# Kernel tuning notes

Hardware: AMD Instinct MI355X
Metric: run time of the kernel (lower is better)

## Reference

```python
import jax, jax.numpy as jnp
import numpy as np

N_NODES = 10000
N_EDGES = 640000
D_FEAT = 128
N_CLASSES = 40


def setup_inputs() -> dict:
    key = jax.random.key(0)
    k1, k2, k3, k4 = jax.random.split(key, 4)
    x = jax.random.normal(k1, (N_NODES, D_FEAT), dtype=jnp.float32)
    edge_index = jax.random.randint(k2, (2, N_EDGES), 0, N_NODES, dtype=jnp.int64)
    # SAGEConv params: lin_l (neighbor path, with bias), lin_r (root path, no bias)
    W_l = jax.random.normal(k3, (D_FEAT, N_CLASSES), dtype=jnp.float32) / np.sqrt(D_FEAT)
    b_l = jnp.zeros((N_CLASSES,), dtype=jnp.float32)
    W_r = jax.random.normal(k4, (D_FEAT, N_CLASSES), dtype=jnp.float32) / np.sqrt(D_FEAT)
    return {"x": x, "edge_index": edge_index, "W_l": W_l, "b_l": b_l, "W_r": W_r}


def reference(x, edge_index, W_l, b_l, W_r):
    # SAGEConv(aggr='max'): gather source features, scatter-max into destinations
    src, dst = edge_index[0], edge_index[1]
    msgs = x[src]                                        # [E, F] gather
    agg = jax.ops.segment_max(msgs, dst, num_segments=x.shape[0])  # [N, F]
    # nodes with no incoming edges: PyG fills with 0
    agg = jnp.where(jnp.isneginf(agg), 0.0, agg)
    out = agg @ W_l + b_l + x @ W_r                      # [N, C]
    return jax.nn.log_softmax(out, axis=1)
```

## Files before the change

### kernel.cpp

```cpp
#include <hip/hip_runtime.h>
#include <hip/hip_bf16.h>
#include <math.h>

#define D_FEAT 128
#define N_CLASSES 40
#define CAP 128

#define CNT_PAD_INTS (10000 * 16)
#define XB_BYTES (10000 * D_FEAT * 2)
#define CNT_BYTES (CNT_PAD_INTS * 4)

typedef int v4i __attribute__((ext_vector_type(4)));


extern "C" __global__ void __launch_bounds__(256)
gnn_cvt(const float* __restrict__ x, __hip_bfloat16* __restrict__ xb,
        int* __restrict__ cnt, int n4)
{
    int t = blockIdx.x * 256 + threadIdx.x;
    if (t < CNT_PAD_INTS / 4) {
        reinterpret_cast<v4i*>(cnt)[t] = (v4i){0, 0, 0, 0};
    }
    if (t >= n4) return;
    float4 v = reinterpret_cast<const float4*>(x)[t];
    __hip_bfloat16 o[4];
    o[0] = __float2bfloat16(v.x);
    o[1] = __float2bfloat16(v.y);
    o[2] = __float2bfloat16(v.z);
    o[3] = __float2bfloat16(v.w);
    *reinterpret_cast<uint2*>(xb + (size_t)t * 4) = *reinterpret_cast<uint2*>(o);
}

extern "C" __global__ void __launch_bounds__(256)
gnn_bucketize(const int* __restrict__ src, const int* __restrict__ dst,
              int* __restrict__ cnt, unsigned short* __restrict__ bucket,
              int n_edges4)
{
    int t = blockIdx.x * 256 + threadIdx.x;
    if (t >= n_edges4) return;
    v4i s4 = __builtin_nontemporal_load(reinterpret_cast<const v4i*>(src) + t);
    v4i d4 = __builtin_nontemporal_load(reinterpret_cast<const v4i*>(dst) + t);
    int p0 = atomicAdd(&cnt[d4.x << 4], 1);
    int p1 = atomicAdd(&cnt[d4.y << 4], 1);
    int p2 = atomicAdd(&cnt[d4.z << 4], 1);
    int p3 = atomicAdd(&cnt[d4.w << 4], 1);
    if (p0 < CAP) bucket[(size_t)d4.x * CAP + p0] = (unsigned short)s4.x;
    if (p1 < CAP) bucket[(size_t)d4.y * CAP + p1] = (unsigned short)s4.y;
    if (p2 < CAP) bucket[(size_t)d4.z * CAP + p2] = (unsigned short)s4.z;
    if (p3 < CAP) bucket[(size_t)d4.w * CAP + p3] = (unsigned short)s4.w;
}

extern "C" __global__ void __launch_bounds__(256)
gnn_fused(const float* __restrict__ x, const __hip_bfloat16* __restrict__ xb,
          const int* __restrict__ cnt, const unsigned short* __restrict__ bucket,
          const float* __restrict__ W_l, const float* __restrict__ b_l,
          const float* __restrict__ W_r,
          float* __restrict__ out, int n_nodes)
{
    __shared__ float sa[4][D_FEAT];
    __shared__ float sx[4][D_FEAT];

    const int wave = threadIdx.x >> 6;
    const int lane = threadIdx.x & 63;
    const int node = blockIdx.x * 4 + wave;
    const bool valid = (node < n_nodes);

    const int sub = lane >> 4;
    const int q   = lane & 15;
    const int c8  = q * 8;

    int deg = 0;
    if (valid) deg = min(cnt[node << 4], CAP);

    float acc[8];
    #pragma unroll
    for (int i = 0; i < 8; ++i) acc[i] = -INFINITY;

    const unsigned short* brow = bucket + (size_t)node * CAP;

    for (int base = 0; base < deg; base += 64) {
        const int nb = min(64, deg - base);
        int myid = brow[base + min(lane, nb - 1)];

        if (nb == 64) {
            #pragma unroll
            for (int k = 0; k < 64; k += 16) {
                int ss[4];
                #pragma unroll
                for (int j = 0; j < 4; ++j) ss[j] = __shfl(myid, k + 4 * j + sub, 64);
                uint4 vv[4];
                #pragma unroll
                for (int j = 0; j < 4; ++j)
                    vv[j] = *reinterpret_cast<const uint4*>(xb + (size_t)ss[j] * D_FEAT + c8);
                #pragma unroll
                for (int j = 0; j < 4; ++j) {
                    const unsigned int* u = &vv[j].x;
                    #pragma unroll
                    for (int w = 0; w < 4; ++w) {
                        acc[2*w]   = fmaxf(acc[2*w],   __uint_as_float(u[w] << 16));
                        acc[2*w+1] = fmaxf(acc[2*w+1], __uint_as_float(u[w] & 0xffff0000u));
                    }
                }
            }
        } else {
            for (int k = 0; k < nb; k += 8) {
                int e0 = min(k + sub, nb - 1);
                int e1 = min(k + 4 + sub, nb - 1);
                int s0 = __shfl(myid, e0, 64);
                int s1 = __shfl(myid, e1, 64);
                uint4 v0 = *reinterpret_cast<const uint4*>(xb + (size_t)s0 * D_FEAT + c8);
                uint4 v1 = *reinterpret_cast<const uint4*>(xb + (size_t)s1 * D_FEAT + c8);
                const unsigned int* u0 = &v0.x;
                const unsigned int* u1 = &v1.x;
                #pragma unroll
                for (int w = 0; w < 4; ++w) {
                    acc[2*w]   = fmaxf(acc[2*w],   __uint_as_float(u0[w] << 16));
                    acc[2*w+1] = fmaxf(acc[2*w+1], __uint_as_float(u0[w] & 0xffff0000u));
                    acc[2*w]   = fmaxf(acc[2*w],   __uint_as_float(u1[w] << 16));
                    acc[2*w+1] = fmaxf(acc[2*w+1], __uint_as_float(u1[w] & 0xffff0000u));
                }
            }
        }
    }

    #pragma unroll
    for (int i = 0; i < 8; ++i) {
        acc[i] = fmaxf(acc[i], __shfl_xor(acc[i], 16, 64));
        acc[i] = fmaxf(acc[i], __shfl_xor(acc[i], 32, 64));
    }
    if (deg == 0) {
        #pragma unroll
        for (int i = 0; i < 8; ++i) acc[i] = 0.0f;
    }

    if (valid) {
        if (sub == 0) {
            #pragma unroll
            for (int i = 0; i < 8; ++i) sa[wave][c8 + i] = acc[i];
        }
        if (lane < 32) {
            *reinterpret_cast<float4*>(&sx[wave][lane * 4]) =
                *reinterpret_cast<const float4*>(x + (size_t)node * D_FEAT + lane * 4);
        }
    }

    float o = 0.0f;
    if (valid && lane < N_CLASSES) {
        o = b_l[lane];
        #pragma unroll 8
        for (int f = 0; f < D_FEAT; ++f) {
            o = fmaf(sa[wave][f], W_l[f * N_CLASSES + lane], o);
            o = fmaf(sx[wave][f], W_r[f * N_CLASSES + lane], o);
        }
    }

    float mm = (valid && lane < N_CLASSES) ? o : -INFINITY;
    #pragma unroll
    for (int off = 32; off > 0; off >>= 1) mm = fmaxf(mm, __shfl_xor(mm, off, 64));
    float ex = (valid && lane < N_CLASSES) ? expf(o - mm) : 0.0f;
    float ss = ex;
    #pragma unroll
    for (int off = 32; off > 0; off >>= 1) ss += __shfl_xor(ss, off, 64);

    if (valid && lane < N_CLASSES)
        out[(size_t)node * N_CLASSES + lane] = o - mm - logf(ss);
}

extern "C" void kernel_launch(void* const* d_in, const int* in_sizes, int n_in,
                              void* d_out, int out_size, void* d_ws, size_t ws_size,
                              hipStream_t stream) {
    const float* x   = (const float*)d_in[0];
    const int*   ei  = (const int*)d_in[1];
    const float* W_l = (const float*)d_in[2];
    const float* b_l = (const float*)d_in[3];
    const float* W_r = (const float*)d_in[4];
    float* out = (float*)d_out;

    const int n_nodes = in_sizes[0] / D_FEAT;
    const int n_edges = in_sizes[1] / 2;
    const int* src = ei;
    const int* dst = ei + n_edges;

    char* w = (char*)d_ws;
    __hip_bfloat16* xb = (__hip_bfloat16*)w;
    int* cnt = (int*)(w + XB_BYTES);
    unsigned short* bucket = (unsigned short*)(w + XB_BYTES + CNT_BYTES);

    {
        int n4 = n_nodes * D_FEAT / 4;
        int blocks = (n4 + 255) / 256;
        gnn_cvt<<<blocks, 256, 0, stream>>>(x, xb, cnt, n4);
    }
    {
        int n_edges4 = n_edges / 4;
        int blocks = (n_edges4 + 255) / 256;
        gnn_bucketize<<<blocks, 256, 0, stream>>>(src, dst, cnt, bucket, n_edges4);
    }
    {
        int blocks = (n_nodes + 3) / 4;
        gnn_fused<<<blocks, 256, 0, stream>>>(x, xb, cnt, bucket, W_l, b_l, W_r,
                                              out, n_nodes);
    }
}
```

Baseline: 70.07 us.

## Switch gathered features to fp16 with packed max and dot2 projection

```diff
diff --git a/kernel.cpp b/kernel.cpp
--- a/kernel.cpp
+++ b/kernel.cpp
@@ -1,5 +1,4 @@
 #include <hip/hip_runtime.h>
-#include <hip/hip_bf16.h>
 #include <math.h>
 
 #define D_FEAT 128
@@ -7,28 +6,50 @@
 #define CAP 128
 
 #define CNT_PAD_INTS (10000 * 16)
-#define XB_BYTES (10000 * D_FEAT * 2)
+#define XH_BYTES (10000 * D_FEAT * 2)
 #define CNT_BYTES (CNT_PAD_INTS * 4)
+#define WPK_U32 (64 * N_CLASSES)
 
 typedef int v4i __attribute__((ext_vector_type(4)));
+typedef _Float16 h2 __attribute__((ext_vector_type(2)));
+
+static __device__ __forceinline__ unsigned int pkmax(unsigned int a, unsigned int b) {
+    unsigned int d;
+    asm("v_pk_max_f16 %0, %1, %2" : "=v"(d) : "v"(a), "v"(b));
+    return d;
+}
+static __device__ __forceinline__ float fdot2(unsigned int a, unsigned int b, float c) {
+    return __builtin_amdgcn_fdot2(__builtin_bit_cast(h2, a),
+                                  __builtin_bit_cast(h2, b), c, false);
+}
+static __device__ __forceinline__ unsigned short f2h(float f) {
+    return __builtin_bit_cast(unsigned short, (_Float16)f);
+}
 
 
 extern "C" __global__ void __launch_bounds__(256)
-gnn_cvt(const float* __restrict__ x, __hip_bfloat16* __restrict__ xb,
-        int* __restrict__ cnt, int n4)
+gnn_cvt(const float* __restrict__ x, unsigned int* __restrict__ xh,
+        int* __restrict__ cnt,
+        const float* __restrict__ W_l, const float* __restrict__ W_r,
+        unsigned int* __restrict__ Wlpk, unsigned int* __restrict__ Wrpk, int n4)
 {
     int t = blockIdx.x * 256 + threadIdx.x;
     if (t < CNT_PAD_INTS / 4) {
         reinterpret_cast<v4i*>(cnt)[t] = (v4i){0, 0, 0, 0};
     }
+    if (t < WPK_U32) {
+        int f2 = t / N_CLASSES, c = t % N_CLASSES;
+        Wlpk[t] = (unsigned int)f2h(W_l[(2 * f2) * N_CLASSES + c])
+                | ((unsigned int)f2h(W_l[(2 * f2 + 1) * N_CLASSES + c]) << 16);
+        Wrpk[t] = (unsigned int)f2h(W_r[(2 * f2) * N_CLASSES + c])
+                | ((unsigned int)f2h(W_r[(2 * f2 + 1) * N_CLASSES + c]) << 16);
+    }
     if (t >= n4) return;
     float4 v = reinterpret_cast<const float4*>(x)[t];
-    __hip_bfloat16 o[4];
-    o[0] = __float2bfloat16(v.x);
-    o[1] = __float2bfloat16(v.y);
-    o[2] = __float2bfloat16(v.z);
-    o[3] = __float2bfloat16(v.w);
-    *reinterpret_cast<uint2*>(xb + (size_t)t * 4) = *reinterpret_cast<uint2*>(o);
+    uint2 o;
+    o.x = (unsigned int)f2h(v.x) | ((unsigned int)f2h(v.y) << 16);
+    o.y = (unsigned int)f2h(v.z) | ((unsigned int)f2h(v.w) << 16);
+    reinterpret_cast<uint2*>(xh)[t] = o;
 }
 
 extern "C" __global__ void __launch_bounds__(256)
@@ -51,14 +72,14 @@
 }
 
 extern "C" __global__ void __launch_bounds__(256)
-gnn_fused(const float* __restrict__ x, const __hip_bfloat16* __restrict__ xb,
+gnn_fused(const unsigned int* __restrict__ xh,
           const int* __restrict__ cnt, const unsigned short* __restrict__ bucket,
-          const float* __restrict__ W_l, const float* __restrict__ b_l,
-          const float* __restrict__ W_r,
+          const unsigned int* __restrict__ Wlpk, const unsigned int* __restrict__ Wrpk,
+          const float* __restrict__ b_l,
           float* __restrict__ out, int n_nodes)
 {
-    __shared__ float sa[4][D_FEAT];
-    __shared__ float sx[4][D_FEAT];
+    __shared__ unsigned int sa2[4][64];
+    __shared__ unsigned int sx2[4][64];
 
     const int wave = threadIdx.x >> 6;
     const int lane = threadIdx.x & 63;
@@ -67,16 +88,16 @@
 
     const int sub = lane >> 4;
     const int q   = lane & 15;
-    const int c8  = q * 8;
 
     int deg = 0;
     if (valid) deg = min(cnt[node << 4], CAP);
 
-    float acc[8];
-    #pragma unroll
-    for (int i = 0; i < 8; ++i) acc[i] = -INFINITY;
+    unsigned int acc2[4];
+    #pragma unroll
+    for (int i = 0; i < 4; ++i) acc2[i] = 0xFC00FC00u;
 
     const unsigned short* brow = bucket + (size_t)node * CAP;
+    const uint4* xh4 = reinterpret_cast<const uint4*>(xh);
 
     for (int base = 0; base < deg; base += 64) {
         const int nb = min(64, deg - base);
@@ -90,16 +111,12 @@
                 for (int j = 0; j < 4; ++j) ss[j] = __shfl(myid, k + 4 * j + sub, 64);
                 uint4 vv[4];
                 #pragma unroll
-                for (int j = 0; j < 4; ++j)
-                    vv[j] = *reinterpret_cast<const uint4*>(xb + (size_t)ss[j] * D_FEAT + c8);
+                for (int j = 0; j < 4; ++j) vv[j] = xh4[ss[j] * 16 + q];
                 #pragma unroll
                 for (int j = 0; j < 4; ++j) {
                     const unsigned int* u = &vv[j].x;
                     #pragma unroll
-                    for (int w = 0; w < 4; ++w) {
-                        acc[2*w]   = fmaxf(acc[2*w],   __uint_as_float(u[w] << 16));
-                        acc[2*w+1] = fmaxf(acc[2*w+1], __uint_as_float(u[w] & 0xffff0000u));
-                    }
+                    for (int w = 0; w < 4; ++w) acc2[w] = pkmax(acc2[w], u[w]);
                 }
             }
         } else {
@@ -108,49 +125,57 @@
                 int e1 = min(k + 4 + sub, nb - 1);
                 int s0 = __shfl(myid, e0, 64);
                 int s1 = __shfl(myid, e1, 64);
-                uint4 v0 = *reinterpret_cast<const uint4*>(xb + (size_t)s0 * D_FEAT + c8);
-                uint4 v1 = *reinterpret_cast<const uint4*>(xb + (size_t)s1 * D_FEAT + c8);
+                uint4 v0 = xh4[s0 * 16 + q];
+                uint4 v1 = xh4[s1 * 16 + q];
                 const unsigned int* u0 = &v0.x;
                 const unsigned int* u1 = &v1.x;
                 #pragma unroll
                 for (int w = 0; w < 4; ++w) {
-                    acc[2*w]   = fmaxf(acc[2*w],   __uint_as_float(u0[w] << 16));
-                    acc[2*w+1] = fmaxf(acc[2*w+1], __uint_as_float(u0[w] & 0xffff0000u));
-                    acc[2*w]   = fmaxf(acc[2*w],   __uint_as_float(u1[w] << 16));
-                    acc[2*w+1] = fmaxf(acc[2*w+1], __uint_as_float(u1[w] & 0xffff0000u));
+                    acc2[w] = pkmax(acc2[w], u0[w]);
+                    acc2[w] = pkmax(acc2[w], u1[w]);
                 }
             }
         }
     }
 
     #pragma unroll
-    for (int i = 0; i < 8; ++i) {
-        acc[i] = fmaxf(acc[i], __shfl_xor(acc[i], 16, 64));
-        acc[i] = fmaxf(acc[i], __shfl_xor(acc[i], 32, 64));
+    for (int i = 0; i < 4; ++i) {
+        acc2[i] = pkmax(acc2[i], (unsigned int)__shfl_xor((int)acc2[i], 16, 64));
+        acc2[i] = pkmax(acc2[i], (unsigned int)__shfl_xor((int)acc2[i], 32, 64));
     }
     if (deg == 0) {
         #pragma unroll
-        for (int i = 0; i < 8; ++i) acc[i] = 0.0f;
+        for (int i = 0; i < 4; ++i) acc2[i] = 0u;
     }
 
     if (valid) {
         if (sub == 0) {
-            #pragma unroll
-            for (int i = 0; i < 8; ++i) sa[wave][c8 + i] = acc[i];
-        }
-        if (lane < 32) {
-            *reinterpret_cast<float4*>(&sx[wave][lane * 4]) =
-                *reinterpret_cast<const float4*>(x + (size_t)node * D_FEAT + lane * 4);
+            uint4 w4;
+            w4.x = acc2[0]; w4.y = acc2[1]; w4.z = acc2[2]; w4.w = acc2[3];
+            *reinterpret_cast<uint4*>(&sa2[wave][q * 4]) = w4;
+        }
+        if (lane < 16) {
+            reinterpret_cast<uint4*>(sx2[wave])[lane] = xh4[node * 16 + lane];
         }
     }
 
     float o = 0.0f;
     if (valid && lane < N_CLASSES) {
         o = b_l[lane];
-        #pragma unroll 8
-        for (int f = 0; f < D_FEAT; ++f) {
-            o = fmaf(sa[wave][f], W_l[f * N_CLASSES + lane], o);
-            o = fmaf(sx[wave][f], W_r[f * N_CLASSES + lane], o);
+        const uint4* a4 = reinterpret_cast<const uint4*>(sa2[wave]);
+        const uint4* x4 = reinterpret_cast<const uint4*>(sx2[wave]);
+        #pragma unroll 4
+        for (int i = 0; i < 16; ++i) {
+            uint4 a  = a4[i];
+            uint4 xx = x4[i];
+            const unsigned int* ua = &a.x;
+            const unsigned int* ux = &xx.x;
+            #pragma unroll
+            for (int j = 0; j < 4; ++j) {
+                int f2 = i * 4 + j;
+                o = fdot2(ua[j], Wlpk[f2 * N_CLASSES + lane], o);
+                o = fdot2(ux[j], Wrpk[f2 * N_CLASSES + lane], o);
+            }
         }
     }
 
@@ -182,14 +207,17 @@
     const int* dst = ei + n_edges;
 
     char* w = (char*)d_ws;
-    __hip_bfloat16* xb = (__hip_bfloat16*)w;
-    int* cnt = (int*)(w + XB_BYTES);
-    unsigned short* bucket = (unsigned short*)(w + XB_BYTES + CNT_BYTES);
+    unsigned int* xh = (unsigned int*)w;
+    int* cnt = (int*)(w + XH_BYTES);
+    unsigned int* Wlpk = (unsigned int*)(w + XH_BYTES + CNT_BYTES);
+    unsigned int* Wrpk = Wlpk + WPK_U32;
+    unsigned short* bucket = (unsigned short*)(w + XH_BYTES + CNT_BYTES
+                                               + 2 * WPK_U32 * 4);
 
     {
         int n4 = n_nodes * D_FEAT / 4;
         int blocks = (n4 + 255) / 256;
-        gnn_cvt<<<blocks, 256, 0, stream>>>(x, xb, cnt, n4);
+        gnn_cvt<<<blocks, 256, 0, stream>>>(x, xh, cnt, W_l, W_r, Wlpk, Wrpk, n4);
     }
     {
         int n_edges4 = n_edges / 4;
@@ -198,7 +226,7 @@
     }
     {
         int blocks = (n_nodes + 3) / 4;
-        gnn_fused<<<blocks, 256, 0, stream>>>(x, xb, cnt, bucket, W_l, b_l, W_r,
+        gnn_fused<<<blocks, 256, 0, stream>>>(xh, cnt, bucket, Wlpk, Wrpk, b_l,
                                               out, n_nodes);
     }
 }
```

Result: faster. 59.93 us (-14.5%).
